# Optimization experiments

Hardware: AMD Instinct MI355X
Metric: run time of the kernel (lower is better)

Reference implementation:

```python
import jax, jax.numpy as jnp
import numpy as np

P_K = 3  # patch kernel size
MV_SCALE = 32.0  # flow scale from STN: u/w*2*32


def unfold3(x):
    # torch.nn.Unfold(kernel_size=3, padding=1, stride=1), channel-major ordering
    B, C, H, W = x.shape
    xp = jnp.pad(x, ((0, 0), (0, 0), (1, 1), (1, 1)))
    # index = c*9 + i*3 + j, matching torch Unfold layout
    patches = jnp.stack([xp[:, :, i:i + H, j:j + W]
                         for i in range(P_K) for j in range(P_K)], axis=2)
    return patches  # [B, C, 9, H, W]


def bilinear_sample(img, gx, gy):
    # grid_sample, mode=bilinear, padding_mode=border, align_corners=True
    # img: [B, Cp, H, W]; gx, gy: [B, H, W] in [-1, 1]
    B, Cp, H, W = img.shape
    x = (gx + 1.0) * 0.5 * (W - 1)
    y = (gy + 1.0) * 0.5 * (H - 1)
    x0 = jnp.floor(x)
    y0 = jnp.floor(y)
    wx = (x - x0)[:, None]  # [B,1,H,W]
    wy = (y - y0)[:, None]
    x0i = jnp.clip(x0.astype(jnp.int32), 0, W - 1)
    x1i = jnp.clip(x0i + 1, 0, W - 1)
    y0i = jnp.clip(y0.astype(jnp.int32), 0, H - 1)
    y1i = jnp.clip(y0i + 1, 0, H - 1)
    imgf = img.reshape(B, Cp, H * W)

    def gather(yi, xi):
        idx = (yi * W + xi).reshape(B, -1)  # [B, H*W]
        out = jax.vmap(lambda im, ix: im[:, ix])(imgf, idx)
        return out.reshape(B, Cp, H, W)

    v00 = gather(y0i, x0i)
    v01 = gather(y0i, x1i)
    v10 = gather(y1i, x0i)
    v11 = gather(y1i, x1i)
    return (v00 * (1 - wx) * (1 - wy) + v01 * wx * (1 - wy)
            + v10 * (1 - wx) * wy + v11 * wx * wy)


def setup_inputs() -> dict:
    key = jax.random.key(0)
    ks = jax.random.split(key, 8)
    B, C, H, W = 4, 64, 128, 128
    nf = 64
    cin = nf * P_K * P_K * 2  # 1152
    inp = {
        'nbh_fea': jax.random.normal(ks[0], (B, C, H, W), jnp.float32),
        'cen_fea': jax.random.normal(ks[1], (B, C, H, W), jnp.float32),
        'mv': jax.random.normal(ks[2], (B, 2, H, W), jnp.float32),
        'w1': jax.random.normal(ks[3], (nf, cin), jnp.float32) * 0.02,
        'b1': jnp.zeros((nf,), jnp.float32),
        'w2': jax.random.normal(ks[4], (P_K * P_K, nf), jnp.float32) * 0.05,
        'b2': jnp.zeros((P_K * P_K,), jnp.float32),
    }
    return inp


def reference(nbh_fea, cen_fea, mv, w1, b1, w2, b2):
    B, C, H, W = cen_fea.shape
    K2 = P_K * P_K
    nbh_p = unfold3(nbh_fea).reshape(B, C * K2, H, W)
    cen_p = unfold3(cen_fea).reshape(B, C * K2, H, W)
    # identity mesh in [-1,1], xy indexing (x along W, y along H)
    xv, yv = jnp.meshgrid(jnp.linspace(-1.0, 1.0, W), jnp.linspace(-1.0, 1.0, H))
    u = mv[:, 0] / W * 2.0 * MV_SCALE
    v = mv[:, 1] / H * 2.0 * MV_SCALE
    gx = jnp.clip(xv[None] + u, -1.0, 1.0)
    gy = jnp.clip(yv[None] + v, -1.0, 1.0)
    aligned = bilinear_sample(nbh_p, gx, gy)  # [B, C*9, H, W]
    fuse = jnp.concatenate([aligned, cen_p], axis=1)  # [B, 2*C*9, H, W]
    h1 = jnp.einsum('bchw,oc->bohw', fuse, w1) + b1[None, :, None, None]
    h1 = jnp.where(h1 >= 0, h1, 0.1 * h1)  # LeakyReLU(0.1)
    h2 = jnp.einsum('bchw,oc->bohw', h1, w2) + b2[None, :, None, None]
    attn = jax.nn.softmax(h2, axis=1)  # [B, 9, H, W]
    out = jnp.mean(aligned.reshape(B, C, K2, H, W) * attn[:, None], axis=2)
    return out  # [B, C, H, W]
```

## Files before the change

### kernel.cpp

```cpp
#include <hip/hip_runtime.h>

#define B_   4
#define H_   128
#define W_   128
#define HW_  (H_*W_)
#define CIN_ 1152
#define CP   72

typedef __attribute__((ext_vector_type(8))) short short8;
typedef __attribute__((ext_vector_type(4))) float floatx4;
typedef unsigned short u16;
typedef unsigned int   u32;

__device__ __forceinline__ float bf2f(u16 u){ union{u32 i; float f;} v; v.i=((u32)u)<<16; return v.f; }
__device__ __forceinline__ u16 f2bf(float f){ union{float fl; u32 i;} v; v.fl=f; u32 lsb=(v.i>>16)&1u; v.i += 0x7fffu + lsb; return (u16)(v.i>>16); }

__global__ void k_prep_w(const float* __restrict__ w1,
                         u16* __restrict__ WtA, u16* __restrict__ WtB){
    int o = blockIdx.x, sel = blockIdx.y, k = threadIdx.x;
    int c = k & 63, ij = k >> 6;
    float v = w1[(long)o*CIN_ + sel*576 + c*9 + ij];
    u16* dst = sel ? WtB : WtA;
    dst[o*576 + ij*64 + c] = f2bf(v);
}

__global__ __launch_bounds__(256) void k_t_fwd(
        const float* __restrict__ nbh, const float* __restrict__ cen,
        u16* __restrict__ nbhT, u16* __restrict__ cenT){
    __shared__ u16 tile[64*68];
    int px0 = blockIdx.x * 64;
    int b   = blockIdx.y;
    const float* src = blockIdx.z ? cen : nbh;
    u16* dst         = blockIdx.z ? cenT : nbhT;
    int t  = threadIdx.x;
    int hi = t >> 4, seg = t & 15;
    #pragma unroll
    for (int p = 0; p < 4; ++p){
        int c = p*16 + hi;
        float4 v = *reinterpret_cast<const float4*>(&src[(size_t)(b*64 + c)*HW_ + px0 + seg*4]);
        u16 pk[4] = { f2bf(v.x), f2bf(v.y), f2bf(v.z), f2bf(v.w) };
        *reinterpret_cast<uint2*>(&tile[c*68 + seg*4]) = *reinterpret_cast<uint2*>(pk);
    }
    __syncthreads();
    #pragma unroll
    for (int p = 0; p < 4; ++p){
        int px = p*16 + hi;
        int cg = seg*4;
        u16 pk[4] = { tile[cg*68+px], tile[(cg+1)*68+px], tile[(cg+2)*68+px], tile[(cg+3)*68+px] };
        *reinterpret_cast<uint2*>(&dst[(size_t)(b*HW_ + px0 + px)*64 + cg]) = *reinterpret_cast<uint2*>(pk);
    }
}

__global__ __launch_bounds__(256) void k_conv(
        const u16* __restrict__ nbhT, const u16* __restrict__ cenT,
        const u16* __restrict__ WtA, const u16* __restrict__ WtB,
        u16* __restrict__ convA, u16* __restrict__ convB){
    __shared__ __align__(16) u16 patch[6*66*CP];
    __shared__ __align__(16) u16 wall[9*64*64];
    int x0  = blockIdx.x * 64;
    int y0  = blockIdx.y * 4;
    int b   = blockIdx.z >> 1;
    int sel = blockIdx.z & 1;
    const u16* src = sel ? cenT : nbhT;
    const u16* wt  = sel ? WtB : WtA;
    u16* dst       = sel ? convB : convA;
    int tid = threadIdx.x;

    for (int q = tid; q < 9*64*8; q += 256){
        int row = q >> 3, c8 = q & 7;
        int o = row & 63, ij = row >> 6;
        *reinterpret_cast<uint4*>(&wall[row*64 + c8*8]) =
            *reinterpret_cast<const uint4*>(&wt[o*576 + ij*64 + c8*8]);
    }
    #pragma unroll
    for (int r = 0; r < 6; ++r){
        int gy = y0 - 1 + r;
        bool rok = (gy >= 0) && (gy < H_);
        for (int q = tid; q < 66*8; q += 256){
            int col = q >> 3, c8 = q & 7;
            int gx = x0 - 1 + col;
            uint4 val = make_uint4(0u,0u,0u,0u);
            if (rok && gx >= 0 && gx < W_)
                val = *reinterpret_cast<const uint4*>(&src[((size_t)(b*HW_ + gy*W_ + gx))*64 + c8*8]);
            *reinterpret_cast<uint4*>(&patch[(r*66 + col)*CP + c8*8]) = val;
        }
    }
    __syncthreads();

    int lane = tid & 63;
    int m    = lane & 15;
    int qd   = lane >> 4;
    int w    = tid >> 6;

    floatx4 acc[4][4] = {};
    #pragma unroll
    for (int ij = 0; ij < 9; ++ij){
        const int i = ij/3, j = ij%3;
        #pragma unroll
        for (int s = 0; s < 2; ++s){
            int c0 = s*32 + qd*8;
            short8 bv[4];
            #pragma unroll
            for (int nt = 0; nt < 4; ++nt)
                bv[nt] = *reinterpret_cast<const short8*>(&wall[(ij*64 + nt*16 + m)*64 + c0]);
            #pragma unroll
            for (int mt = 0; mt < 4; ++mt){
                short8 av = *reinterpret_cast<const short8*>(
                    &patch[((w + i)*66 + mt*16 + m + j)*CP + c0]);
                #pragma unroll
                for (int nt = 0; nt < 4; ++nt)
                    acc[mt][nt] = __builtin_amdgcn_mfma_f32_16x16x32_bf16(av, bv[nt], acc[mt][nt], 0, 0, 0);
            }
        }
    }

    size_t base = ((size_t)(b*HW_ + (y0 + w)*W_ + x0))*64;
    #pragma unroll
    for (int mt = 0; mt < 4; ++mt)
        #pragma unroll
        for (int nt = 0; nt < 4; ++nt)
            #pragma unroll
            for (int r = 0; r < 4; ++r){
                int px = mt*16 + qd*4 + r;
                int o  = nt*16 + m;
                dst[base + (size_t)px*64 + o] = f2bf(acc[mt][nt][r]);
            }
}

__device__ __forceinline__ float fetchA(float am, int lane, int i, int j){
    bool ok = (i >= 1) & (i <= 3) & (j >= 1) & (j <= 3);
    int k = (i-1)*3 + (j-1);
    k = min(max(k, 0), 8);
    float v = __shfl(am, (lane & 48) | k, 64);
    return ok ? v : 0.f;
}

__global__ __launch_bounds__(256) void k_attn(
        const u16* __restrict__ nbhT,
        const u16* __restrict__ convA, const u16* __restrict__ convB,
        const float* __restrict__ mv,
        const float* __restrict__ b1, const float* __restrict__ w2,
        const float* __restrict__ b2, float* __restrict__ out){
    __shared__ __align__(16) int cwoff[64*16*2];
    __shared__ float otile[64*66];
    int tid  = threadIdx.x;
    int lane = tid & 63;
    int w    = tid >> 6;
    int m    = lane & 15;
    int qd   = lane >> 4;
    int pix0 = blockIdx.x*64;
    int b    = pix0 >> 14;
    int y    = (pix0 >> 7) & 127;
    int xblk = pix0 & 127;
    int x    = xblk + w*16 + m;
    size_t pb = (size_t)b*HW_*64;
    const u16* nb = nbhT + pb;

    float u  = mv[(long)(b*2  )*HW_ + y*W_ + x] * 0.5f;
    float v  = mv[(long)(b*2+1)*HW_ + y*W_ + x] * 0.5f;
    float gx = fminf(fmaxf(-1.0f + x*(2.0f/127.0f) + u, -1.f), 1.f);
    float gy = fminf(fmaxf(-1.0f + y*(2.0f/127.0f) + v, -1.f), 1.f);
    float sx = (gx + 1.f) * 63.5f;
    float sy = (gy + 1.f) * 63.5f;
    float x0f = floorf(sx), y0f = floorf(sy);
    float wx = sx - x0f,    wy = sy - y0f;
    int x0i = min(max((int)x0f, 0), W_-1);
    int y0i = min(max((int)y0f, 0), H_-1);
    int x1i = min(x0i+1, W_-1);
    int y1i = min(y0i+1, H_-1);
    float wx0 = 1.f - wx, wy0 = 1.f - wy;

    short8 av[2];
    #pragma unroll
    for (int s = 0; s < 2; ++s){
        int c0 = s*32 + qd*8;
        short8 q00 = *reinterpret_cast<const short8*>(&convA[pb + (size_t)(y0i*W_+x0i)*64 + c0]);
        short8 q01 = *reinterpret_cast<const short8*>(&convA[pb + (size_t)(y0i*W_+x1i)*64 + c0]);
        short8 q10 = *reinterpret_cast<const short8*>(&convA[pb + (size_t)(y1i*W_+x0i)*64 + c0]);
        short8 q11 = *reinterpret_cast<const short8*>(&convA[pb + (size_t)(y1i*W_+x1i)*64 + c0]);
        short8 qc  = *reinterpret_cast<const short8*>(&convB[pb + (size_t)(y*W_+x)*64 + c0]);
        short8 h;
        #pragma unroll
        for (int j = 0; j < 8; ++j){
            float t = wy0*(wx0*bf2f((u16)q00[j]) + wx*bf2f((u16)q01[j]))
                    + wy *(wx0*bf2f((u16)q10[j]) + wx*bf2f((u16)q11[j]))
                    + bf2f((u16)qc[j]) + b1[c0+j];
            t = t >= 0.f ? t : 0.1f*t;
            h[j] = (short)f2bf(t);
        }
        av[s] = h;
    }
    short8 bv[2];
    #pragma unroll
    for (int s = 0; s < 2; ++s){
        int c0 = s*32 + qd*8;
        short8 t = {0,0,0,0,0,0,0,0};
        if (m < 9){
            #pragma unroll
            for (int j = 0; j < 8; ++j) t[j] = (short)f2bf(w2[m*64 + c0 + j]);
        }
        bv[s] = t;
    }
    floatx4 C = {0.f,0.f,0.f,0.f};
    C = __builtin_amdgcn_mfma_f32_16x16x32_bf16(av[0], bv[0], C, 0, 0, 0);
    C = __builtin_amdgcn_mfma_f32_16x16x32_bf16(av[1], bv[1], C, 0, 0, 0);

    float b2k = (m < 9) ? b2[m] : 0.f;
    float am[4];
    #pragma unroll
    for (int r = 0; r < 4; ++r){
        float e  = C[r] + b2k;
        float mx = (m < 9) ? e : -3.0e38f;
        #pragma unroll
        for (int d = 1; d < 16; d <<= 1) mx = fmaxf(mx, __shfl_xor(mx, d, 64));
        float a = (m < 9) ? __expf(e - mx) : 0.f;
        float s = a;
        #pragma unroll
        for (int d = 1; d < 16; d <<= 1) s += __shfl_xor(s, d, 64);
        am[r] = a / (9.f * s);
    }

    int gpack = x0i | (y0i << 8) | ((y1i > y0i) ? 0x10000 : 0) | ((x1i > x0i) ? 0x20000 : 0);
    int at = m >> 2, bt = m & 3;
    #pragma unroll
    for (int r = 0; r < 4; ++r){
        int p   = qd*4 + r;
        int src = (lane & 48) | p;
        float wxp = __shfl(wx, src, 64);
        float wyp = __shfl(wy, src, 64);
        int   gp  = __shfl(gpack, src, 64);
        int x0p = gp & 255, y0p = (gp >> 8) & 255;
        int dy1 = (gp >> 16) & 1, dx1 = (gp >> 17) & 1;
        float wx0p = 1.f - wxp, wy0p = 1.f - wyp;
        int ia = dy1 ? at : at+1;
        int jb = dx1 ? bt : bt+1;
        float cw = wy0p*wx0p*fetchA(am[r], lane, at+1, bt+1)
                 + wy0p*wxp *fetchA(am[r], lane, at+1, jb)
                 + wyp *wx0p*fetchA(am[r], lane, ia,   bt+1)
                 + wyp *wxp *fetchA(am[r], lane, ia,   jb);
        int ry = y0p - 1 + at, rx = x0p - 1 + bt;
        bool ok = (ry >= 0) & (ry < H_) & (rx >= 0) & (rx < W_);
        int2 pr;
        pr.x = __float_as_int(ok ? cw : 0.f);
        pr.y = ok ? (ry*W_ + rx)*64 : 0;
        *reinterpret_cast<int2*>(&cwoff[((w*16 + p)*16 + m)*2]) = pr;
    }

    for (int s = 0; s < 16; ++s){
        int slot = w*16 + s;
        const int4* pr4 = reinterpret_cast<const int4*>(&cwoff[slot*32]);
        float acc = 0.f;
        #pragma unroll
        for (int k = 0; k < 8; ++k){
            int4 p = pr4[k];
            acc += __int_as_float(p.x) * bf2f(nb[(size_t)p.y + lane]);
            acc += __int_as_float(p.z) * bf2f(nb[(size_t)p.w + lane]);
        }
        otile[lane*66 + slot] = acc;
    }
    __syncthreads();

    int px = tid & 63;
    #pragma unroll
    for (int p = 0; p < 16; ++p){
        int c = w*16 + p;
        out[(size_t)(b*64 + c)*HW_ + y*W_ + xblk + px] = otile[c*66 + px];
    }
}

extern "C" void kernel_launch(void* const* d_in, const int* in_sizes, int n_in,
                              void* d_out, int out_size, void* d_ws, size_t ws_size,
                              hipStream_t stream){
    const float* nbh = (const float*)d_in[0];
    const float* cen = (const float*)d_in[1];
    const float* mv  = (const float*)d_in[2];
    const float* w1  = (const float*)d_in[3];
    const float* b1  = (const float*)d_in[4];
    const float* w2  = (const float*)d_in[5];
    const float* b2  = (const float*)d_in[6];
    float* out = (float*)d_out;

    const size_t IMG = (size_t)B_*HW_*64;
    char* ws = (char*)d_ws;
    u16* WtA   = (u16*)ws;
    u16* WtB   = WtA + 64*576;
    u16* convA = (u16*)(ws + 147456);
    u16* convB = convA + IMG;
    u16* nbhT  = convB + IMG;
    u16* cenT  = nbhT  + IMG;

    hipLaunchKernelGGL(k_prep_w, dim3(64,2),    dim3(576), 0, stream, w1, WtA, WtB);
    hipLaunchKernelGGL(k_t_fwd,  dim3(256,4,2), dim3(256), 0, stream, nbh, cen, nbhT, cenT);
    hipLaunchKernelGGL(k_conv,   dim3(2,32,8),  dim3(256), 0, stream,
                       nbhT, cenT, WtA, WtB, convA, convB);
    hipLaunchKernelGGL(k_attn,   dim3(1024),    dim3(256), 0, stream,
                       nbhT, convA, convB, mv, b1, w2, b2, out);
}
```

Baseline: 153.2 us.

## Stream conv weights per tap and read patches from global; widen attn blocks

```diff
diff --git a/kernel.cpp b/kernel.cpp
--- a/kernel.cpp
+++ b/kernel.cpp
@@ -5,7 +5,6 @@
 #define W_   128
 #define HW_  (H_*W_)
 #define CIN_ 1152
-#define CP   72
 
 typedef __attribute__((ext_vector_type(8))) short short8;
 typedef __attribute__((ext_vector_type(4))) float floatx4;
@@ -55,8 +54,7 @@
         const u16* __restrict__ nbhT, const u16* __restrict__ cenT,
         const u16* __restrict__ WtA, const u16* __restrict__ WtB,
         u16* __restrict__ convA, u16* __restrict__ convB){
-    __shared__ __align__(16) u16 patch[6*66*CP];
-    __shared__ __align__(16) u16 wall[9*64*64];
+    __shared__ __align__(16) u16 wtile[2][64*72];
     int x0  = blockIdx.x * 64;
     int y0  = blockIdx.y * 4;
     int b   = blockIdx.z >> 1;
@@ -64,57 +62,57 @@
     const u16* src = sel ? cenT : nbhT;
     const u16* wt  = sel ? WtB : WtA;
     u16* dst       = sel ? convB : convA;
-    int tid = threadIdx.x;
-
-    for (int q = tid; q < 9*64*8; q += 256){
-        int row = q >> 3, c8 = q & 7;
-        int o = row & 63, ij = row >> 6;
-        *reinterpret_cast<uint4*>(&wall[row*64 + c8*8]) =
-            *reinterpret_cast<const uint4*>(&wt[o*576 + ij*64 + c8*8]);
-    }
-    #pragma unroll
-    for (int r = 0; r < 6; ++r){
-        int gy = y0 - 1 + r;
-        bool rok = (gy >= 0) && (gy < H_);
-        for (int q = tid; q < 66*8; q += 256){
-            int col = q >> 3, c8 = q & 7;
-            int gx = x0 - 1 + col;
-            uint4 val = make_uint4(0u,0u,0u,0u);
-            if (rok && gx >= 0 && gx < W_)
-                val = *reinterpret_cast<const uint4*>(&src[((size_t)(b*HW_ + gy*W_ + gx))*64 + c8*8]);
-            *reinterpret_cast<uint4*>(&patch[(r*66 + col)*CP + c8*8]) = val;
-        }
-    }
-    __syncthreads();
-
-    int lane = tid & 63;
-    int m    = lane & 15;
-    int qd   = lane >> 4;
-    int w    = tid >> 6;
-
+    int tid  = threadIdx.x;
+    int lane = tid & 63, m = lane & 15, qd = lane >> 4, w = tid >> 6;
+    int gy   = y0 + w;
+
+    for (int q = tid; q < 64*8; q += 256){
+        int o = q >> 3, c8 = q & 7;
+        *reinterpret_cast<uint4*>(&wtile[0][o*72 + c8*8]) =
+            *reinterpret_cast<const uint4*>(&wt[o*576 + c8*8]);
+    }
+
+    const size_t rowstride = (size_t)W_*64;
+    const u16* img = src + (size_t)b*HW_*64;
     floatx4 acc[4][4] = {};
+
     #pragma unroll
     for (int ij = 0; ij < 9; ++ij){
+        __syncthreads();
+        if (ij < 8){
+            int nij = ij + 1;
+            for (int q = tid; q < 64*8; q += 256){
+                int o = q >> 3, c8 = q & 7;
+                *reinterpret_cast<uint4*>(&wtile[nij & 1][o*72 + c8*8]) =
+                    *reinterpret_cast<const uint4*>(&wt[o*576 + nij*64 + c8*8]);
+            }
+        }
         const int i = ij/3, j = ij%3;
-        #pragma unroll
-        for (int s = 0; s < 2; ++s){
-            int c0 = s*32 + qd*8;
-            short8 bv[4];
-            #pragma unroll
-            for (int nt = 0; nt < 4; ++nt)
-                bv[nt] = *reinterpret_cast<const short8*>(&wall[(ij*64 + nt*16 + m)*64 + c0]);
-            #pragma unroll
-            for (int mt = 0; mt < 4; ++mt){
-                short8 av = *reinterpret_cast<const short8*>(
-                    &patch[((w + i)*66 + mt*16 + m + j)*CP + c0]);
+        int ry = gy + i - 1;
+        if (ry >= 0 && ry < H_){
+            const u16* srow = img + (size_t)ry*rowstride;
+            #pragma unroll
+            for (int s = 0; s < 2; ++s){
+                int c0 = s*32 + qd*8;
+                short8 bv[4];
                 #pragma unroll
                 for (int nt = 0; nt < 4; ++nt)
-                    acc[mt][nt] = __builtin_amdgcn_mfma_f32_16x16x32_bf16(av, bv[nt], acc[mt][nt], 0, 0, 0);
-            }
-        }
-    }
-
-    size_t base = ((size_t)(b*HW_ + (y0 + w)*W_ + x0))*64;
+                    bv[nt] = *reinterpret_cast<const short8*>(&wtile[ij & 1][(nt*16 + m)*72 + c0]);
+                #pragma unroll
+                for (int mt = 0; mt < 4; ++mt){
+                    int gx = x0 - 1 + mt*16 + m + j;
+                    short8 av = {0,0,0,0,0,0,0,0};
+                    if (gx >= 0 && gx < W_)
+                        av = *reinterpret_cast<const short8*>(&srow[(size_t)gx*64 + c0]);
+                    #pragma unroll
+                    for (int nt = 0; nt < 4; ++nt)
+                        acc[mt][nt] = __builtin_amdgcn_mfma_f32_16x16x32_bf16(av, bv[nt], acc[mt][nt], 0, 0, 0);
+                }
+            }
+        }
+    }
+
+    size_t base = ((size_t)(b*HW_ + gy*W_ + x0))*64;
     #pragma unroll
     for (int mt = 0; mt < 4; ++mt)
         #pragma unroll
@@ -135,7 +133,7 @@
     return ok ? v : 0.f;
 }
 
-__global__ __launch_bounds__(256) void k_attn(
+__global__ __launch_bounds__(512) void k_attn(
         const u16* __restrict__ nbhT,
         const u16* __restrict__ convA, const u16* __restrict__ convB,
         const float* __restrict__ mv,
@@ -152,118 +150,128 @@
     int b    = pix0 >> 14;
     int y    = (pix0 >> 7) & 127;
     int xblk = pix0 & 127;
-    int x    = xblk + w*16 + m;
     size_t pb = (size_t)b*HW_*64;
     const u16* nb = nbhT + pb;
 
-    float u  = mv[(long)(b*2  )*HW_ + y*W_ + x] * 0.5f;
-    float v  = mv[(long)(b*2+1)*HW_ + y*W_ + x] * 0.5f;
-    float gx = fminf(fmaxf(-1.0f + x*(2.0f/127.0f) + u, -1.f), 1.f);
-    float gy = fminf(fmaxf(-1.0f + y*(2.0f/127.0f) + v, -1.f), 1.f);
-    float sx = (gx + 1.f) * 63.5f;
-    float sy = (gy + 1.f) * 63.5f;
-    float x0f = floorf(sx), y0f = floorf(sy);
-    float wx = sx - x0f,    wy = sy - y0f;
-    int x0i = min(max((int)x0f, 0), W_-1);
-    int y0i = min(max((int)y0f, 0), H_-1);
-    int x1i = min(x0i+1, W_-1);
-    int y1i = min(y0i+1, H_-1);
-    float wx0 = 1.f - wx, wy0 = 1.f - wy;
-
-    short8 av[2];
-    #pragma unroll
-    for (int s = 0; s < 2; ++s){
-        int c0 = s*32 + qd*8;
-        short8 q00 = *reinterpret_cast<const short8*>(&convA[pb + (size_t)(y0i*W_+x0i)*64 + c0]);
-        short8 q01 = *reinterpret_cast<const short8*>(&convA[pb + (size_t)(y0i*W_+x1i)*64 + c0]);
-        short8 q10 = *reinterpret_cast<const short8*>(&convA[pb + (size_t)(y1i*W_+x0i)*64 + c0]);
-        short8 q11 = *reinterpret_cast<const short8*>(&convA[pb + (size_t)(y1i*W_+x1i)*64 + c0]);
-        short8 qc  = *reinterpret_cast<const short8*>(&convB[pb + (size_t)(y*W_+x)*64 + c0]);
-        short8 h;
-        #pragma unroll
-        for (int j = 0; j < 8; ++j){
-            float t = wy0*(wx0*bf2f((u16)q00[j]) + wx*bf2f((u16)q01[j]))
-                    + wy *(wx0*bf2f((u16)q10[j]) + wx*bf2f((u16)q11[j]))
-                    + bf2f((u16)qc[j]) + b1[c0+j];
-            t = t >= 0.f ? t : 0.1f*t;
-            h[j] = (short)f2bf(t);
-        }
-        av[s] = h;
-    }
-    short8 bv[2];
-    #pragma unroll
-    for (int s = 0; s < 2; ++s){
-        int c0 = s*32 + qd*8;
-        short8 t = {0,0,0,0,0,0,0,0};
-        if (m < 9){
-            #pragma unroll
-            for (int j = 0; j < 8; ++j) t[j] = (short)f2bf(w2[m*64 + c0 + j]);
-        }
-        bv[s] = t;
-    }
-    floatx4 C = {0.f,0.f,0.f,0.f};
-    C = __builtin_amdgcn_mfma_f32_16x16x32_bf16(av[0], bv[0], C, 0, 0, 0);
-    C = __builtin_amdgcn_mfma_f32_16x16x32_bf16(av[1], bv[1], C, 0, 0, 0);
-
-    float b2k = (m < 9) ? b2[m] : 0.f;
-    float am[4];
-    #pragma unroll
-    for (int r = 0; r < 4; ++r){
-        float e  = C[r] + b2k;
-        float mx = (m < 9) ? e : -3.0e38f;
-        #pragma unroll
-        for (int d = 1; d < 16; d <<= 1) mx = fmaxf(mx, __shfl_xor(mx, d, 64));
-        float a = (m < 9) ? __expf(e - mx) : 0.f;
-        float s = a;
-        #pragma unroll
-        for (int d = 1; d < 16; d <<= 1) s += __shfl_xor(s, d, 64);
-        am[r] = a / (9.f * s);
-    }
-
-    int gpack = x0i | (y0i << 8) | ((y1i > y0i) ? 0x10000 : 0) | ((x1i > x0i) ? 0x20000 : 0);
-    int at = m >> 2, bt = m & 3;
-    #pragma unroll
-    for (int r = 0; r < 4; ++r){
-        int p   = qd*4 + r;
-        int src = (lane & 48) | p;
-        float wxp = __shfl(wx, src, 64);
-        float wyp = __shfl(wy, src, 64);
-        int   gp  = __shfl(gpack, src, 64);
-        int x0p = gp & 255, y0p = (gp >> 8) & 255;
-        int dy1 = (gp >> 16) & 1, dx1 = (gp >> 17) & 1;
-        float wx0p = 1.f - wxp, wy0p = 1.f - wyp;
-        int ia = dy1 ? at : at+1;
-        int jb = dx1 ? bt : bt+1;
-        float cw = wy0p*wx0p*fetchA(am[r], lane, at+1, bt+1)
-                 + wy0p*wxp *fetchA(am[r], lane, at+1, jb)
-                 + wyp *wx0p*fetchA(am[r], lane, ia,   bt+1)
-                 + wyp *wxp *fetchA(am[r], lane, ia,   jb);
-        int ry = y0p - 1 + at, rx = x0p - 1 + bt;
-        bool ok = (ry >= 0) & (ry < H_) & (rx >= 0) & (rx < W_);
-        int2 pr;
-        pr.x = __float_as_int(ok ? cw : 0.f);
-        pr.y = ok ? (ry*W_ + rx)*64 : 0;
-        *reinterpret_cast<int2*>(&cwoff[((w*16 + p)*16 + m)*2]) = pr;
-    }
-
-    for (int s = 0; s < 16; ++s){
-        int slot = w*16 + s;
-        const int4* pr4 = reinterpret_cast<const int4*>(&cwoff[slot*32]);
-        float acc = 0.f;
+    if (w < 4){
+        int x = xblk + w*16 + m;
+        float u  = mv[(long)(b*2  )*HW_ + y*W_ + x] * 0.5f;
+        float v  = mv[(long)(b*2+1)*HW_ + y*W_ + x] * 0.5f;
+        float gx = fminf(fmaxf(-1.0f + x*(2.0f/127.0f) + u, -1.f), 1.f);
+        float gy = fminf(fmaxf(-1.0f + y*(2.0f/127.0f) + v, -1.f), 1.f);
+        float sx = (gx + 1.f) * 63.5f;
+        float sy = (gy + 1.f) * 63.5f;
+        float x0f = floorf(sx), y0f = floorf(sy);
+        float wx = sx - x0f,    wy = sy - y0f;
+        int x0i = min(max((int)x0f, 0), W_-1);
+        int y0i = min(max((int)y0f, 0), H_-1);
+        int x1i = min(x0i+1, W_-1);
+        int y1i = min(y0i+1, H_-1);
+        float wx0 = 1.f - wx, wy0 = 1.f - wy;
+
+        short8 av[2];
+        #pragma unroll
+        for (int s = 0; s < 2; ++s){
+            int c0 = s*32 + qd*8;
+            short8 q00 = *reinterpret_cast<const short8*>(&convA[pb + (size_t)(y0i*W_+x0i)*64 + c0]);
+            short8 q01 = *reinterpret_cast<const short8*>(&convA[pb + (size_t)(y0i*W_+x1i)*64 + c0]);
+            short8 q10 = *reinterpret_cast<const short8*>(&convA[pb + (size_t)(y1i*W_+x0i)*64 + c0]);
+            short8 q11 = *reinterpret_cast<const short8*>(&convA[pb + (size_t)(y1i*W_+x1i)*64 + c0]);
+            short8 qc  = *reinterpret_cast<const short8*>(&convB[pb + (size_t)(y*W_+x)*64 + c0]);
+            short8 h;
+            #pragma unroll
+            for (int j = 0; j < 8; ++j){
+                float t = wy0*(wx0*bf2f((u16)q00[j]) + wx*bf2f((u16)q01[j]))
+                        + wy *(wx0*bf2f((u16)q10[j]) + wx*bf2f((u16)q11[j]))
+                        + bf2f((u16)qc[j]) + b1[c0+j];
+                t = t >= 0.f ? t : 0.1f*t;
+                h[j] = (short)f2bf(t);
+            }
+            av[s] = h;
+        }
+        short8 bv[2];
+        #pragma unroll
+        for (int s = 0; s < 2; ++s){
+            int c0 = s*32 + qd*8;
+            short8 t = {0,0,0,0,0,0,0,0};
+            if (m < 9){
+                #pragma unroll
+                for (int j = 0; j < 8; ++j) t[j] = (short)f2bf(w2[m*64 + c0 + j]);
+            }
+            bv[s] = t;
+        }
+        floatx4 C = {0.f,0.f,0.f,0.f};
+        C = __builtin_amdgcn_mfma_f32_16x16x32_bf16(av[0], bv[0], C, 0, 0, 0);
+        C = __builtin_amdgcn_mfma_f32_16x16x32_bf16(av[1], bv[1], C, 0, 0, 0);
+
+        float b2k = (m < 9) ? b2[m] : 0.f;
+        float am[4];
+        #pragma unroll
+        for (int r = 0; r < 4; ++r){
+            float e  = C[r] + b2k;
+            float mx = (m < 9) ? e : -3.0e38f;
+            #pragma unroll
+            for (int d = 1; d < 16; d <<= 1) mx = fmaxf(mx, __shfl_xor(mx, d, 64));
+            float a = (m < 9) ? __expf(e - mx) : 0.f;
+            float s = a;
+            #pragma unroll
+            for (int d = 1; d < 16; d <<= 1) s += __shfl_xor(s, d, 64);
+            am[r] = a / (9.f * s);
+        }
+
+        int gpack = x0i | (y0i << 8) | ((y1i > y0i) ? 0x10000 : 0) | ((x1i > x0i) ? 0x20000 : 0);
+        int at = m >> 2, bt = m & 3;
+        #pragma unroll
+        for (int r = 0; r < 4; ++r){
+            int p   = qd*4 + r;
+            int src = (lane & 48) | p;
+            float wxp = __shfl(wx, src, 64);
+            float wyp = __shfl(wy, src, 64);
+            int   gp  = __shfl(gpack, src, 64);
+            int x0p = gp & 255, y0p = (gp >> 8) & 255;
+            int dy1 = (gp >> 16) & 1, dx1 = (gp >> 17) & 1;
+            float wx0p = 1.f - wxp, wy0p = 1.f - wyp;
+            int ia = dy1 ? at : at+1;
+            int jb = dx1 ? bt : bt+1;
+            float cw = wy0p*wx0p*fetchA(am[r], lane, at+1, bt+1)
+                     + wy0p*wxp *fetchA(am[r], lane, at+1, jb)
+                     + wyp *wx0p*fetchA(am[r], lane, ia,   bt+1)
+                     + wyp *wxp *fetchA(am[r], lane, ia,   jb);
+            int ry = y0p - 1 + at, rx = x0p - 1 + bt;
+            bool ok = (ry >= 0) & (ry < H_) & (rx >= 0) & (rx < W_);
+            int2 pr;
+            pr.x = __float_as_int(ok ? cw : 0.f);
+            pr.y = ok ? (ry*W_ + rx)*64 : 0;
+            *reinterpret_cast<int2*>(&cwoff[((w*16 + p)*16 + m)*2]) = pr;
+        }
+    }
+    __syncthreads();
+
+    const u16* nbl = nb + lane;
+    #pragma unroll
+    for (int sp = 0; sp < 8; sp += 2){
+        int slot0 = w*8 + sp;
+        const int4* a4 = reinterpret_cast<const int4*>(&cwoff[slot0*32]);
+        const int4* b4 = reinterpret_cast<const int4*>(&cwoff[(slot0+1)*32]);
+        float acc0 = 0.f, acc1 = 0.f;
         #pragma unroll
         for (int k = 0; k < 8; ++k){
-            int4 p = pr4[k];
-            acc += __int_as_float(p.x) * bf2f(nb[(size_t)p.y + lane]);
-            acc += __int_as_float(p.z) * bf2f(nb[(size_t)p.w + lane]);
-        }
-        otile[lane*66 + slot] = acc;
+            int4 pa = a4[k];
+            int4 pbv = b4[k];
+            acc0 += __int_as_float(pa.x)  * bf2f(nbl[(size_t)pa.y]);
+            acc1 += __int_as_float(pbv.x) * bf2f(nbl[(size_t)pbv.y]);
+            acc0 += __int_as_float(pa.z)  * bf2f(nbl[(size_t)pa.w]);
+            acc1 += __int_as_float(pbv.z) * bf2f(nbl[(size_t)pbv.w]);
+        }
+        otile[lane*66 + slot0]     = acc0;
+        otile[lane*66 + slot0 + 1] = acc1;
     }
     __syncthreads();
 
-    int px = tid & 63;
-    #pragma unroll
-    for (int p = 0; p < 16; ++p){
-        int c = w*16 + p;
+    int px = lane;
+    #pragma unroll
+    for (int p = 0; p < 8; ++p){
+        int c = w*8 + p;
         out[(size_t)(b*64 + c)*HW_ + y*W_ + xblk + px] = otile[c*66 + px];
     }
 }
@@ -293,6 +301,6 @@
     hipLaunchKernelGGL(k_t_fwd,  dim3(256,4,2), dim3(256), 0, stream, nbh, cen, nbhT, cenT);
     hipLaunchKernelGGL(k_conv,   dim3(2,32,8),  dim3(256), 0, stream,
                        nbhT, cenT, WtA, WtB, convA, convB);
-    hipLaunchKernelGGL(k_attn,   dim3(1024),    dim3(256), 0, stream,
+    hipLaunchKernelGGL(k_attn,   dim3(1024),    dim3(512), 0, stream,
                        nbhT, convA, convB, mv, b1, w2, b2, out);
 }
```

Result: faster. 144.5 us (-5.7%).
